# Optimization experiments

Hardware: AMD Instinct MI355X
Metric: run time of the kernel (lower is better)

Reference implementation:

```python
import jax, jax.numpy as jnp
import numpy as np

HOPS = 3
VOCAB = 100000
E = 128   # embedding_dim == hidden_size
H = 128
B = 16
S = 2048  # memory slots
M = 4     # tokens per memory cell
NE = 4000 # lang.n_entities
NR = 200  # lang.n_relations
PAD = 1   # PAD_token


def _linear_params(key, out_dim, in_dim):
    kw, kb = jax.random.split(key)
    lim = 1.0 / np.sqrt(in_dim)
    W = jax.random.uniform(kw, (out_dim, in_dim), jnp.float32, -lim, lim)
    b = jax.random.uniform(kb, (out_dim,), jnp.float32, -lim, lim)
    return W, b


def setup_inputs():
    key = jax.random.key(0)
    ks = jax.random.split(key, 10)
    story = jax.random.randint(ks[0], (B, S, M), 0, VOCAB)
    lengths = jax.random.randint(ks[1], (B,), S // 2, S + 1)
    hidden = jax.random.normal(ks[2], (B, H), jnp.float32)
    global_pointer = jax.random.uniform(ks[3], (B, S), dtype=jnp.float32)
    # (hops+1) memory embedding tables, N(0, 0.1), padding row zeroed
    C = jax.random.normal(ks[4], (HOPS + 1, VOCAB, E), jnp.float32) * 0.1
    C = C.at[:, PAD, :].set(0.0)
    Wm, Wb = _linear_params(ks[5], H, H)        # self.W
    W1w, W1b = _linear_params(ks[6], 2, H)      # structure type
    W3w, W3b = _linear_params(ks[7], NE, H)     # query entity h
    W4w, W4b = _linear_params(ks[8], NR, H)     # query entity t
    return dict(story=story, lengths=lengths, hidden=hidden,
                global_pointer=global_pointer, C=C,
                Wm=Wm, Wb=Wb, W1w=W1w, W1b=W1b,
                W3w=W3w, W3b=W3b, W4w=W4w, W4b=W4b,
                is_decoding=0)


def gumbel_hard(logits, key, tau=1.0):
    u = jax.random.uniform(key, logits.shape, logits.dtype, 1e-10, 1.0)
    g = -jnp.log(-jnp.log(u))
    y = jax.nn.softmax((logits + g) / tau, axis=-1)
    hard = jax.nn.one_hot(jnp.argmax(y, axis=-1), y.shape[-1], dtype=y.dtype)
    # straight-through estimator
    return hard - jax.lax.stop_gradient(y) + y


def reference(story, lengths, hidden, global_pointer, C,
              Wm, Wb, W1w, W1b, W3w, W3b, W4w, W4b, is_decoding):
    del global_pointer, is_decoding  # decoding branch not exercised (is_decoding=False)
    h = hidden @ Wm.T + Wb  # [B, H]

    gkey = jax.random.key(42)
    k1, k2, k3 = jax.random.split(gkey, 3)
    sp = h @ W1w.T + W1b
    sp_action = gumbel_hard(sp, k1)
    qh = h @ W3w.T + W3b
    qh_action = gumbel_hard(qh, k2)
    qt = h @ W4w.T + W4b
    qt_action = gumbel_hard(qt, k3)

    # multi-hop memory attention (dropout in eval mode -> identity)
    u = h
    prob_logit = None
    for hop in range(HOPS):
        embed_A = jnp.take(C[hop], story, axis=0).sum(axis=2)      # [B,S,E]
        prob_logit = jnp.einsum('bse,be->bs', embed_A, u)          # [B,S]
        prob = jax.nn.softmax(prob_logit, axis=1)
        embed_C = jnp.take(C[hop + 1], story, axis=0).sum(axis=2)  # [B,S,E]
        u = u + jnp.einsum('bse,bs->be', embed_C, prob)

    ret = jax.nn.sigmoid(prob_logit)
    mask = jnp.arange(S)[None, :] < lengths[:, None]
    masked_prob = jnp.where(mask, ret, 0.0)
    return (sp, sp_action, qh, qh_action, qt, qt_action, masked_prob)
```

## Files before the change

### kernel.cpp

```cpp
#include <hip/hip_runtime.h>
#include <hip/hip_bf16.h>
#include <stdint.h>

typedef __hip_bfloat16 bf16;

#define VOCABN 100000
#define EDIM 128
#define BN 16
#define SN 2048

#define H_OFF    0
#define U_OFF    2048
#define L0_OFF   4096
#define DUP_OFF  36864
#define PBV_OFF  69648
#define PBI_OFF  70848
#define G_OFF    73728

__host__ __device__ inline void tf2x32(uint32_t k0, uint32_t k1,
                                       uint32_t x0, uint32_t x1,
                                       uint32_t* o0, uint32_t* o1) {
  const uint32_t rotA[4] = {13u, 15u, 26u, 6u};
  const uint32_t rotB[4] = {17u, 29u, 16u, 24u};
  uint32_t ks0 = k0, ks1 = k1, ks2 = k0 ^ k1 ^ 0x1BD11BDAu;
  x0 += ks0; x1 += ks1;
#pragma unroll
  for (int g = 0; g < 5; ++g) {
    const uint32_t* r = (g & 1) ? rotB : rotA;
#pragma unroll
    for (int i = 0; i < 4; ++i) {
      x0 += x1;
      x1 = (x1 << r[i]) | (x1 >> (32u - r[i]));
      x1 ^= x0;
    }
    uint32_t a0 = (g % 3 == 0) ? ks1 : ((g % 3 == 1) ? ks2 : ks0);
    uint32_t a1 = (g % 3 == 0) ? ks2 : ((g % 3 == 1) ? ks0 : ks1);
    x0 += a0;
    x1 += a1 + (uint32_t)(g + 1);
  }
  *o0 = x0; *o1 = x1;
}

__device__ inline float blo(uint32_t v) { return __uint_as_float(v << 16); }
__device__ inline float bhi(uint32_t v) { return __uint_as_float(v & 0xffff0000u); }
__device__ inline uint16_t f2bu(float f) {
  bf16 h = __float2bfloat16(f);
  uint16_t u; __builtin_memcpy(&u, &h, 2); return u;
}
__device__ inline float gumbel(uint32_t ka, uint32_t kb, uint32_t flat) {
  uint32_t o0, o1;
  tf2x32(ka, kb, 0u, flat, &o0, &o1);
  uint32_t bits = o0 ^ o1;
  float u0 = __uint_as_float((bits >> 9) | 0x3f800000u) - 1.0f;
  float uu = fmaxf(1e-10f, u0 + 1e-10f);
  return -logf(-logf(uu));
}

__global__ void k_h(const float* __restrict__ hidden, const float* __restrict__ Wm,
                    const float* __restrict__ Wb, float* __restrict__ h,
                    float* __restrict__ u) {
  int b = blockIdx.x, j = threadIdx.x;
  const float4* wr = (const float4*)(Wm + (size_t)j * EDIM);
  const float4* hr = (const float4*)(hidden + (size_t)b * EDIM);
  float acc = Wb[j];
#pragma unroll
  for (int i = 0; i < 32; ++i) {
    float4 w4 = wr[i], h4 = hr[i];
    acc += w4.x * h4.x + w4.y * h4.y + w4.z * h4.z + w4.w * h4.w;
  }
  h[b * EDIM + j] = acc;
  u[b * EDIM + j] = acc;
}

__global__ void k_heads(const float* __restrict__ h,
                        const float* __restrict__ W1w, const float* __restrict__ W1b,
                        const float* __restrict__ W3w, const float* __restrict__ W3b,
                        const float* __restrict__ W4w, const float* __restrict__ W4b,
                        float* __restrict__ out, float* __restrict__ pbv,
                        int* __restrict__ pbi,
                        uint32_t k0a, uint32_t k0b, uint32_t k1a, uint32_t k1b,
                        uint32_t k2a, uint32_t k2b) {
  int bid = blockIdx.x, tid = threadIdx.x;
  __shared__ float hb[EDIM];
  __shared__ float sv[256];
  __shared__ int si[256];
  int head, b2, base, cnt, chunk, N;
  const float *W, *bias; size_t lg_off; uint32_t ka, kb;
  if (bid < 400)      { head = 1; b2 = bid / 25; chunk = bid % 25; base = chunk * 160; cnt = 160;
                        W = W3w; bias = W3b; N = 4000; lg_off = 64;     ka = k1a; kb = k1b; }
  else if (bid < 416) { head = 2; b2 = bid - 400; chunk = 0; base = 0; cnt = 200;
                        W = W4w; bias = W4b; N = 200;  lg_off = 128064; ka = k2a; kb = k2b; }
  else                { head = 0; b2 = bid - 416; chunk = 0; base = 0; cnt = 2;
                        W = W1w; bias = W1b; N = 2;    lg_off = 0;      ka = k0a; kb = k0b; }
  if (tid < 128) hb[tid] = h[b2 * EDIM + tid];
  __syncthreads();
  float best = -INFINITY; int bi = 0x7FFFFFFF;
  if (tid < cnt) {
    int c = base + tid;
    const float4* wr = (const float4*)(W + (size_t)c * EDIM);
    const float4* hb4 = (const float4*)hb;
    float acc = bias[c];
#pragma unroll
    for (int i = 0; i < 32; ++i) {
      float4 w4 = wr[i], h4 = hb4[i];
      acc += w4.x * h4.x + w4.y * h4.y + w4.z * h4.z + w4.w * h4.w;
    }
    out[lg_off + (size_t)b2 * N + c] = acc;
    best = acc + gumbel(ka, kb, (uint32_t)(b2 * N + c));
    bi = c;
  }
  sv[tid] = best; si[tid] = bi;
  __syncthreads();
  for (int s2 = 128; s2 > 0; s2 >>= 1) {
    if (tid < s2) {
      float ov = sv[tid + s2]; int oi = si[tid + s2];
      if (ov > sv[tid] || (ov == sv[tid] && oi < si[tid])) { sv[tid] = ov; si[tid] = oi; }
    }
    __syncthreads();
  }
  if (tid == 0) {
    pbv[(head * 16 + b2) * 25 + chunk] = sv[0];
    pbi[(head * 16 + b2) * 25 + chunk] = si[0];
  }
}

__global__ void k_onehot(const float* __restrict__ pbv, const int* __restrict__ pbi,
                         float* __restrict__ out) {
  int g = blockIdx.x * 256 + threadIdx.x;
  if (g >= 67232) return;
  int head, b2, c; size_t off; int nch;
  if (g < 64000)      { head = 1; b2 = g / 4000; c = g % 4000; off = 64064 + g;          nch = 25; }
  else if (g < 67200) { int gg = g - 64000; head = 2; b2 = gg / 200; c = gg % 200; off = 131264 + gg; nch = 1; }
  else                { int gg = g - 67200; head = 0; b2 = gg >> 1; c = gg & 1;   off = 32 + gg;     nch = 1; }
  float bv = -INFINITY; int bi = 0x7FFFFFFF;
  for (int ch = 0; ch < nch; ++ch) {
    float v = pbv[(head * 16 + b2) * 25 + ch];
    int i2 = pbi[(head * 16 + b2) * 25 + ch];
    if (v > bv || (v == bv && i2 < bi)) { bv = v; bi = i2; }
  }
  out[off] = (c == bi) ? 1.0f : 0.0f;
}

__global__ void k_gather_l0(const int* __restrict__ story, const float* __restrict__ C,
                            const float* __restrict__ u, uint32_t* __restrict__ G,
                            float* __restrict__ l0) {
  int wid = (blockIdx.x << 2) | (threadIdx.x >> 6);
  int lane = threadIdx.x & 63;
  int t = wid >> 15;
  int bs = wid & 32767;
  int4 idx = ((const int4*)story)[bs];
  const float2* r0 = (const float2*)(C + ((size_t)t * VOCABN + idx.x) * EDIM);
  const float2* r1 = (const float2*)(C + ((size_t)t * VOCABN + idx.y) * EDIM);
  const float2* r2 = (const float2*)(C + ((size_t)t * VOCABN + idx.z) * EDIM);
  const float2* r3 = (const float2*)(C + ((size_t)t * VOCABN + idx.w) * EDIM);
  float2 a = r0[lane], b = r1[lane], c = r2[lane], d = r3[lane];
  float lo = a.x + b.x + c.x + d.x;
  float hi = a.y + b.y + c.y + d.y;
  if (t == 0) {
    float2 uu = ((const float2*)(u + ((bs >> 11) << 7)))[lane];
    float s = lo * uu.x + hi * uu.y;
#pragma unroll
    for (int off = 32; off > 0; off >>= 1) s += __shfl_xor(s, off, 64);
    if (lane == 0) l0[bs] = s;
  } else {
    G[((size_t)(t - 1) * BN * SN + bs) * 64 + lane] =
        (uint32_t)f2bu(lo) | ((uint32_t)f2bu(hi) << 16);
  }
}

__global__ void __launch_bounds__(256) k_hopB(const uint32_t* __restrict__ Gt,
                                              const float* __restrict__ row_in,
                                              float* __restrict__ dup) {
  const int b = blockIdx.x >> 4, k = blockIdx.x & 15;
  const int tid = threadIdx.x, wave = tid >> 6, lane = tid & 63;
  __shared__ float sr[SN];
  __shared__ float red[4];
  __shared__ float acc[4][EDIM];

  const float4* rin = (const float4*)(row_in + (size_t)b * SN);
  float4* sr4 = (float4*)sr;
  for (int i = tid; i < SN / 4; i += 256) sr4[i] = rin[i];
  __syncthreads();

  float m = -INFINITY;
  for (int i = tid; i < SN; i += 256) m = fmaxf(m, sr[i]);
#pragma unroll
  for (int off = 32; off > 0; off >>= 1) m = fmaxf(m, __shfl_xor(m, off, 64));
  if (lane == 0) red[wave] = m;
  __syncthreads();
  m = fmaxf(fmaxf(red[0], red[1]), fmaxf(red[2], red[3]));

  float s = 0.f;
  for (int i = tid; i < SN; i += 256) s += expf(sr[i] - m);
#pragma unroll
  for (int off = 32; off > 0; off >>= 1) s += __shfl_xor(s, off, 64);
  __syncthreads();
  if (lane == 0) red[wave] = s;
  __syncthreads();
  float invS = 1.0f / (red[0] + red[1] + red[2] + red[3]);

  const uint32_t* Gb = Gt + (size_t)b * SN * 64;
  int sub = lane >> 4, le = lane & 15;
  float a[8] = {0, 0, 0, 0, 0, 0, 0, 0};
#pragma unroll
  for (int it = 0; it < 8; ++it) {
    int cell = k * 128 + wave * 32 + it * 4 + sub;
    uint4 v = *(const uint4*)(Gb + (size_t)cell * 64 + le * 4);
    float pp = expf(sr[cell] - m);
    a[0] += blo(v.x) * pp; a[1] += bhi(v.x) * pp;
    a[2] += blo(v.y) * pp; a[3] += bhi(v.y) * pp;
    a[4] += blo(v.z) * pp; a[5] += bhi(v.z) * pp;
    a[6] += blo(v.w) * pp; a[7] += bhi(v.w) * pp;
  }
#pragma unroll
  for (int j = 0; j < 8; ++j) {
    a[j] += __shfl_xor(a[j], 16, 64);
    a[j] += __shfl_xor(a[j], 32, 64);
  }
  if (lane < 16) {
#pragma unroll
    for (int j = 0; j < 8; ++j) acc[wave][lane * 8 + j] = a[j];
  }
  __syncthreads();
  if (tid < EDIM) {
    float d = (acc[0][tid] + acc[1][tid] + acc[2][tid] + acc[3][tid]) * invS;
    dup[((size_t)b * 16 + k) * EDIM + tid] = d;
  }
}

__global__ void __launch_bounds__(256) k_hopC(const uint32_t* __restrict__ Gt,
                                              const float* __restrict__ dup,
                                              const float* __restrict__ u_in,
                                              float* __restrict__ u_out,
                                              float* __restrict__ row_out,
                                              const int* __restrict__ lengths,
                                              float* __restrict__ out) {
  const int b = blockIdx.x >> 4, k = blockIdx.x & 15;
  const int tid = threadIdx.x, wave = tid >> 6, lane = tid & 63;
  __shared__ float u_l[EDIM];
  if (tid < EDIM) {
    float v = u_in[b * EDIM + tid];
    const float* dp = dup + (size_t)b * 16 * EDIM + tid;
#pragma unroll
    for (int kk = 0; kk < 16; ++kk) v += dp[kk * EDIM];
    u_l[tid] = v;
    if (u_out != nullptr && k == 0) u_out[b * EDIM + tid] = v;
  }
  __syncthreads();

  const uint32_t* Gb = Gt + (size_t)b * SN * 64;
  int sub = lane >> 4, le = lane & 15;
  const float4* u4 = (const float4*)u_l;
  float4 ua = u4[le * 2], ub = u4[le * 2 + 1];
  int len = (lengths != nullptr) ? lengths[b] : 0;
#pragma unroll
  for (int it = 0; it < 8; ++it) {
    int cell = k * 128 + wave * 32 + it * 4 + sub;
    uint4 v = *(const uint4*)(Gb + (size_t)cell * 64 + le * 4);
    float s = blo(v.x) * ua.x + bhi(v.x) * ua.y + blo(v.y) * ua.z + bhi(v.y) * ua.w
            + blo(v.z) * ub.x + bhi(v.z) * ub.y + blo(v.w) * ub.z + bhi(v.w) * ub.w;
#pragma unroll
    for (int off = 8; off > 0; off >>= 1) s += __shfl_xor(s, off, 64);
    if (le == 0) {
      if (row_out != nullptr) {
        row_out[(size_t)b * SN + cell] = s;
      } else {
        out[134464 + (size_t)b * SN + cell] =
            (cell < len) ? 1.0f / (1.0f + expf(-s)) : 0.0f;
      }
    }
  }
}

extern "C" void kernel_launch(void* const* d_in, const int* in_sizes, int n_in,
                              void* d_out, int out_size, void* d_ws, size_t ws_size,
                              hipStream_t stream) {
  const int *story = nullptr, *lengths = nullptr;
  const float *hidden = nullptr, *C = nullptr, *Wm = nullptr, *Wb = nullptr,
              *W1w = nullptr, *W1b = nullptr, *W3w = nullptr, *W3b = nullptr,
              *W4w = nullptr, *W4b = nullptr;
  for (int i = 0; i < n_in; ++i) {
    switch (in_sizes[i]) {
      case 16 * 2048 * 4:    story   = (const int*)d_in[i]; break;
      case 16:               lengths = (const int*)d_in[i]; break;
      case 16 * 128:         hidden  = (const float*)d_in[i]; break;
      case 4 * 100000 * 128: C       = (const float*)d_in[i]; break;
      case 128 * 128:        Wm      = (const float*)d_in[i]; break;
      case 128:              Wb      = (const float*)d_in[i]; break;
      case 2 * 128:          W1w     = (const float*)d_in[i]; break;
      case 2:                W1b     = (const float*)d_in[i]; break;
      case 4000 * 128:       W3w     = (const float*)d_in[i]; break;
      case 4000:             W3b     = (const float*)d_in[i]; break;
      case 200 * 128:        W4w     = (const float*)d_in[i]; break;
      case 200:              W4b     = (const float*)d_in[i]; break;
      default: break;
    }
  }
  float* out = (float*)d_out;
  float* ws  = (float*)d_ws;
  float* h   = ws + H_OFF;
  float* u   = ws + U_OFF;
  float* row = ws + L0_OFF;
  float* dup = ws + DUP_OFF;
  float* pbv = ws + PBV_OFF;
  int*   pbi = (int*)(ws + PBI_OFF);
  uint32_t* G = (uint32_t*)(ws + G_OFF);
  const size_t TSZ = (size_t)BN * SN * 64;

  uint32_t k0a, k0b, k1a, k1b, k2a, k2b;
  tf2x32(0u, 42u, 0u, 0u, &k0a, &k0b);
  tf2x32(0u, 42u, 0u, 1u, &k1a, &k1b);
  tf2x32(0u, 42u, 0u, 2u, &k2a, &k2b);

  k_h<<<BN, 128, 0, stream>>>(hidden, Wm, Wb, h, u);
  k_heads<<<432, 256, 0, stream>>>(h, W1w, W1b, W3w, W3b, W4w, W4b,
                                   out, pbv, pbi, k0a, k0b, k1a, k1b, k2a, k2b);
  k_onehot<<<263, 256, 0, stream>>>(pbv, pbi, out);
  k_gather_l0<<<3 * BN * SN / 4, 256, 0, stream>>>(story, C, u, G, row);

  k_hopB<<<BN * 16, 256, 0, stream>>>(G, row, dup);
  k_hopC<<<BN * 16, 256, 0, stream>>>(G, dup, u, h, row,
                                      nullptr, out);
  k_hopB<<<BN * 16, 256, 0, stream>>>(G + TSZ, row, dup);
  k_hopC<<<BN * 16, 256, 0, stream>>>(G + TSZ, dup, h, nullptr, nullptr,
                                      lengths, out);
}
```

Baseline: 332.9 us.

## Replace per-slot embedding gathers with vocab-wide dot products and scatter-weighted reductions

```diff
diff --git a/kernel.cpp b/kernel.cpp
--- a/kernel.cpp
+++ b/kernel.cpp
@@ -1,21 +1,23 @@
 #include <hip/hip_runtime.h>
 #include <hip/hip_bf16.h>
 #include <stdint.h>
-
-typedef __hip_bfloat16 bf16;
 
 #define VOCABN 100000
 #define EDIM 128
 #define BN 16
 #define SN 2048
+#define VPB 128
+#define NBV 782
 
 #define H_OFF    0
-#define U_OFF    2048
-#define L0_OFF   4096
-#define DUP_OFF  36864
-#define PBV_OFF  69648
-#define PBI_OFF  70848
-#define G_OFF    73728
+#define U0_OFF   2048
+#define U1_OFF   4096
+#define DU_OFF   6144
+#define PS_OFF   10240
+#define PBV_OFF  10368
+#define PBI_OFF  11568
+#define DT_OFF   16384
+#define WT_OFF   1616384
 
 __host__ __device__ inline void tf2x32(uint32_t k0, uint32_t k1,
                                        uint32_t x0, uint32_t x1,
@@ -41,12 +43,6 @@
   *o0 = x0; *o1 = x1;
 }
 
-__device__ inline float blo(uint32_t v) { return __uint_as_float(v << 16); }
-__device__ inline float bhi(uint32_t v) { return __uint_as_float(v & 0xffff0000u); }
-__device__ inline uint16_t f2bu(float f) {
-  bf16 h = __float2bfloat16(f);
-  uint16_t u; __builtin_memcpy(&u, &h, 2); return u;
-}
 __device__ inline float gumbel(uint32_t ka, uint32_t kb, uint32_t flat) {
   uint32_t o0, o1;
   tf2x32(ka, kb, 0u, flat, &o0, &o1);
@@ -141,135 +137,139 @@
   out[off] = (c == bi) ? 1.0f : 0.0f;
 }
 
-__global__ void k_gather_l0(const int* __restrict__ story, const float* __restrict__ C,
-                            const float* __restrict__ u, uint32_t* __restrict__ G,
-                            float* __restrict__ l0) {
-  int wid = (blockIdx.x << 2) | (threadIdx.x >> 6);
-  int lane = threadIdx.x & 63;
-  int t = wid >> 15;
-  int bs = wid & 32767;
-  int4 idx = ((const int4*)story)[bs];
-  const float2* r0 = (const float2*)(C + ((size_t)t * VOCABN + idx.x) * EDIM);
-  const float2* r1 = (const float2*)(C + ((size_t)t * VOCABN + idx.y) * EDIM);
-  const float2* r2 = (const float2*)(C + ((size_t)t * VOCABN + idx.z) * EDIM);
-  const float2* r3 = (const float2*)(C + ((size_t)t * VOCABN + idx.w) * EDIM);
-  float2 a = r0[lane], b = r1[lane], c = r2[lane], d = r3[lane];
-  float lo = a.x + b.x + c.x + d.x;
-  float hi = a.y + b.y + c.y + d.y;
-  if (t == 0) {
-    float2 uu = ((const float2*)(u + ((bs >> 11) << 7)))[lane];
-    float s = lo * uu.x + hi * uu.y;
-#pragma unroll
-    for (int off = 32; off > 0; off >>= 1) s += __shfl_xor(s, off, 64);
-    if (lane == 0) l0[bs] = s;
-  } else {
-    G[((size_t)(t - 1) * BN * SN + bs) * 64 + lane] =
-        (uint32_t)f2bu(lo) | ((uint32_t)f2bu(hi) << 16);
-  }
-}
-
-__global__ void __launch_bounds__(256) k_hopB(const uint32_t* __restrict__ Gt,
-                                              const float* __restrict__ row_in,
-                                              float* __restrict__ dup) {
-  const int b = blockIdx.x >> 4, k = blockIdx.x & 15;
-  const int tid = threadIdx.x, wave = tid >> 6, lane = tid & 63;
-  __shared__ float sr[SN];
+__global__ void __launch_bounds__(256) k_D(const float* __restrict__ Ct,
+                                           const float* __restrict__ u_in,
+                                           const float* __restrict__ du,
+                                           const float* __restrict__ ps,
+                                           int use_du,
+                                           float* __restrict__ u_out,
+                                           float* __restrict__ Dt,
+                                           float* __restrict__ wtz,
+                                           float* __restrict__ duz) {
+  __shared__ __align__(16) float u_s[16][132];
+  __shared__ __align__(16) float r_s[16][132];
+  const int bid = blockIdx.x, tid = threadIdx.x;
+
+  if (wtz) {
+    for (int i = bid * 256 + tid; i < VOCABN * 16; i += NBV * 256) wtz[i] = 0.f;
+  }
+  if (duz && bid == 0) {
+    for (int i = tid; i < 4096; i += 256) duz[i] = 0.f;
+  }
+
+  for (int i = tid; i < 2048; i += 256) {
+    int b = i >> 7, e = i & 127;
+    float v = u_in[i];
+    if (use_du) {
+      float S = 0.f;
+#pragma unroll
+      for (int sl = 0; sl < 8; ++sl) S += ps[b * 8 + sl];
+      v += du[i] * (1.0f / S);
+    }
+    u_s[b][e] = v;
+    if (u_out && bid == 0) u_out[i] = v;
+  }
+
+  const int v0 = bid * VPB;
+  const int vl = tid >> 4, b = tid & 15;
+  for (int r = 0; r < VPB / 16; ++r) {
+    int vr0 = v0 + r * 16;
+    __syncthreads();
+    for (int i = tid; i < 512; i += 256) {
+      int row = i >> 5, c4 = i & 31;
+      float4 val = make_float4(0.f, 0.f, 0.f, 0.f);
+      if (vr0 + row < VOCABN)
+        val = ((const float4*)(Ct + (size_t)(vr0 + row) * EDIM))[c4];
+      *(float4*)&r_s[row][c4 * 4] = val;
+    }
+    __syncthreads();
+    float acc = 0.f;
+    const float4* rr = (const float4*)&r_s[vl][0];
+    const float4* uu = (const float4*)&u_s[b][0];
+#pragma unroll
+    for (int i = 0; i < 32; ++i) {
+      float4 a = rr[i], c = uu[i];
+      acc += a.x * c.x + a.y * c.y + a.z * c.z + a.w * c.w;
+    }
+    int v = vr0 + vl;
+    if (v < VOCABN) Dt[(size_t)v * 16 + b] = acc;
+  }
+}
+
+__global__ void __launch_bounds__(256) k_lscat(const int* __restrict__ story,
+                                               const float* __restrict__ Dt,
+                                               float* __restrict__ wt,
+                                               float* __restrict__ ps) {
+  const int bid = blockIdx.x, tid = threadIdx.x;
+  const int b = bid >> 3, sl = bid & 7;
+  const int s = sl * 256 + tid;
+  const int wave = tid >> 6, lane = tid & 63;
+  int4 tk = ((const int4*)story)[b * SN + s];
+  float l = Dt[(size_t)tk.x * 16 + b] + Dt[(size_t)tk.y * 16 + b]
+          + Dt[(size_t)tk.z * 16 + b] + Dt[(size_t)tk.w * 16 + b];
+  float e = expf(l);
+  atomicAdd(&wt[(size_t)tk.x * 16 + b], e);
+  atomicAdd(&wt[(size_t)tk.y * 16 + b], e);
+  atomicAdd(&wt[(size_t)tk.z * 16 + b], e);
+  atomicAdd(&wt[(size_t)tk.w * 16 + b], e);
+  float sum = e;
+#pragma unroll
+  for (int off = 32; off > 0; off >>= 1) sum += __shfl_xor(sum, off, 64);
   __shared__ float red[4];
-  __shared__ float acc[4][EDIM];
-
-  const float4* rin = (const float4*)(row_in + (size_t)b * SN);
-  float4* sr4 = (float4*)sr;
-  for (int i = tid; i < SN / 4; i += 256) sr4[i] = rin[i];
+  if (lane == 0) red[wave] = sum;
   __syncthreads();
-
-  float m = -INFINITY;
-  for (int i = tid; i < SN; i += 256) m = fmaxf(m, sr[i]);
-#pragma unroll
-  for (int off = 32; off > 0; off >>= 1) m = fmaxf(m, __shfl_xor(m, off, 64));
-  if (lane == 0) red[wave] = m;
-  __syncthreads();
-  m = fmaxf(fmaxf(red[0], red[1]), fmaxf(red[2], red[3]));
-
-  float s = 0.f;
-  for (int i = tid; i < SN; i += 256) s += expf(sr[i] - m);
-#pragma unroll
-  for (int off = 32; off > 0; off >>= 1) s += __shfl_xor(s, off, 64);
-  __syncthreads();
-  if (lane == 0) red[wave] = s;
-  __syncthreads();
-  float invS = 1.0f / (red[0] + red[1] + red[2] + red[3]);
-
-  const uint32_t* Gb = Gt + (size_t)b * SN * 64;
-  int sub = lane >> 4, le = lane & 15;
-  float a[8] = {0, 0, 0, 0, 0, 0, 0, 0};
-#pragma unroll
-  for (int it = 0; it < 8; ++it) {
-    int cell = k * 128 + wave * 32 + it * 4 + sub;
-    uint4 v = *(const uint4*)(Gb + (size_t)cell * 64 + le * 4);
-    float pp = expf(sr[cell] - m);
-    a[0] += blo(v.x) * pp; a[1] += bhi(v.x) * pp;
-    a[2] += blo(v.y) * pp; a[3] += bhi(v.y) * pp;
-    a[4] += blo(v.z) * pp; a[5] += bhi(v.z) * pp;
-    a[6] += blo(v.w) * pp; a[7] += bhi(v.w) * pp;
-  }
-#pragma unroll
-  for (int j = 0; j < 8; ++j) {
-    a[j] += __shfl_xor(a[j], 16, 64);
-    a[j] += __shfl_xor(a[j], 32, 64);
-  }
-  if (lane < 16) {
-#pragma unroll
-    for (int j = 0; j < 8; ++j) acc[wave][lane * 8 + j] = a[j];
-  }
-  __syncthreads();
-  if (tid < EDIM) {
-    float d = (acc[0][tid] + acc[1][tid] + acc[2][tid] + acc[3][tid]) * invS;
-    dup[((size_t)b * 16 + k) * EDIM + tid] = d;
-  }
-}
-
-__global__ void __launch_bounds__(256) k_hopC(const uint32_t* __restrict__ Gt,
-                                              const float* __restrict__ dup,
-                                              const float* __restrict__ u_in,
-                                              float* __restrict__ u_out,
-                                              float* __restrict__ row_out,
+  if (tid == 0) ps[b * 8 + sl] = red[0] + red[1] + red[2] + red[3];
+}
+
+__global__ void __launch_bounds__(256) k_du(const float* __restrict__ Ct,
+                                            const float* __restrict__ wt,
+                                            float* __restrict__ du) {
+  __shared__ __align__(16) float r_s[16][132];
+  __shared__ float w_s[16][17];
+  const int bid = blockIdx.x, tid = threadIdx.x;
+  const int b = tid >> 4, e8 = (tid & 15) * 8;
+  float acc[8] = {0.f, 0.f, 0.f, 0.f, 0.f, 0.f, 0.f, 0.f};
+  const int v0 = bid * VPB;
+  for (int r = 0; r < VPB / 16; ++r) {
+    int vr0 = v0 + r * 16;
+    __syncthreads();
+    for (int i = tid; i < 512; i += 256) {
+      int row = i >> 5, c4 = i & 31;
+      float4 val = make_float4(0.f, 0.f, 0.f, 0.f);
+      if (vr0 + row < VOCABN)
+        val = ((const float4*)(Ct + (size_t)(vr0 + row) * EDIM))[c4];
+      *(float4*)&r_s[row][c4 * 4] = val;
+    }
+    {
+      int row = tid >> 4, bb = tid & 15;
+      w_s[row][bb] = (vr0 + row < VOCABN) ? wt[(size_t)(vr0 + row) * 16 + bb] : 0.f;
+    }
+    __syncthreads();
+#pragma unroll
+    for (int v = 0; v < 16; ++v) {
+      float w = w_s[v][b];
+      const float4* rp = (const float4*)&r_s[v][e8];
+      float4 A = rp[0], Bv = rp[1];
+      acc[0] += w * A.x;  acc[1] += w * A.y;  acc[2] += w * A.z;  acc[3] += w * A.w;
+      acc[4] += w * Bv.x; acc[5] += w * Bv.y; acc[6] += w * Bv.z; acc[7] += w * Bv.w;
+    }
+  }
+#pragma unroll
+  for (int j = 0; j < 8; ++j) atomicAdd(&du[b * EDIM + e8 + j], acc[j]);
+}
+
+__global__ void __launch_bounds__(256) k_lfin(const int* __restrict__ story,
+                                              const float* __restrict__ Dt,
                                               const int* __restrict__ lengths,
                                               float* __restrict__ out) {
-  const int b = blockIdx.x >> 4, k = blockIdx.x & 15;
-  const int tid = threadIdx.x, wave = tid >> 6, lane = tid & 63;
-  __shared__ float u_l[EDIM];
-  if (tid < EDIM) {
-    float v = u_in[b * EDIM + tid];
-    const float* dp = dup + (size_t)b * 16 * EDIM + tid;
-#pragma unroll
-    for (int kk = 0; kk < 16; ++kk) v += dp[kk * EDIM];
-    u_l[tid] = v;
-    if (u_out != nullptr && k == 0) u_out[b * EDIM + tid] = v;
-  }
-  __syncthreads();
-
-  const uint32_t* Gb = Gt + (size_t)b * SN * 64;
-  int sub = lane >> 4, le = lane & 15;
-  const float4* u4 = (const float4*)u_l;
-  float4 ua = u4[le * 2], ub = u4[le * 2 + 1];
-  int len = (lengths != nullptr) ? lengths[b] : 0;
-#pragma unroll
-  for (int it = 0; it < 8; ++it) {
-    int cell = k * 128 + wave * 32 + it * 4 + sub;
-    uint4 v = *(const uint4*)(Gb + (size_t)cell * 64 + le * 4);
-    float s = blo(v.x) * ua.x + bhi(v.x) * ua.y + blo(v.y) * ua.z + bhi(v.y) * ua.w
-            + blo(v.z) * ub.x + bhi(v.z) * ub.y + blo(v.w) * ub.z + bhi(v.w) * ub.w;
-#pragma unroll
-    for (int off = 8; off > 0; off >>= 1) s += __shfl_xor(s, off, 64);
-    if (le == 0) {
-      if (row_out != nullptr) {
-        row_out[(size_t)b * SN + cell] = s;
-      } else {
-        out[134464 + (size_t)b * SN + cell] =
-            (cell < len) ? 1.0f / (1.0f + expf(-s)) : 0.0f;
-      }
-    }
-  }
+  const int bid = blockIdx.x, tid = threadIdx.x;
+  const int b = bid >> 3, sl = bid & 7;
+  const int s = sl * 256 + tid;
+  int4 tk = ((const int4*)story)[b * SN + s];
+  float l = Dt[(size_t)tk.x * 16 + b] + Dt[(size_t)tk.y * 16 + b]
+          + Dt[(size_t)tk.z * 16 + b] + Dt[(size_t)tk.w * 16 + b];
+  int len = lengths[b];
+  out[134464 + (size_t)b * SN + s] = (s < len) ? 1.0f / (1.0f + expf(-l)) : 0.0f;
 }
 
 extern "C" void kernel_launch(void* const* d_in, const int* in_sizes, int n_in,
@@ -299,29 +299,35 @@
   float* out = (float*)d_out;
   float* ws  = (float*)d_ws;
   float* h   = ws + H_OFF;
-  float* u   = ws + U_OFF;
-  float* row = ws + L0_OFF;
-  float* dup = ws + DUP_OFF;
+  float* u0  = ws + U0_OFF;
+  float* u1  = ws + U1_OFF;
+  float* du  = ws + DU_OFF;
+  float* ps  = ws + PS_OFF;
   float* pbv = ws + PBV_OFF;
   int*   pbi = (int*)(ws + PBI_OFF);
-  uint32_t* G = (uint32_t*)(ws + G_OFF);
-  const size_t TSZ = (size_t)BN * SN * 64;
+  float* Dt  = ws + DT_OFF;
+  float* wt  = ws + WT_OFF;
+
+  const float* C0 = C;
+  const float* C1 = C + (size_t)1 * VOCABN * EDIM;
+  const float* C2 = C + (size_t)2 * VOCABN * EDIM;
 
   uint32_t k0a, k0b, k1a, k1b, k2a, k2b;
   tf2x32(0u, 42u, 0u, 0u, &k0a, &k0b);
   tf2x32(0u, 42u, 0u, 1u, &k1a, &k1b);
   tf2x32(0u, 42u, 0u, 2u, &k2a, &k2b);
 
-  k_h<<<BN, 128, 0, stream>>>(hidden, Wm, Wb, h, u);
+  k_h<<<BN, 128, 0, stream>>>(hidden, Wm, Wb, h, u0);
   k_heads<<<432, 256, 0, stream>>>(h, W1w, W1b, W3w, W3b, W4w, W4b,
                                    out, pbv, pbi, k0a, k0b, k1a, k1b, k2a, k2b);
   k_onehot<<<263, 256, 0, stream>>>(pbv, pbi, out);
-  k_gather_l0<<<3 * BN * SN / 4, 256, 0, stream>>>(story, C, u, G, row);
-
-  k_hopB<<<BN * 16, 256, 0, stream>>>(G, row, dup);
-  k_hopC<<<BN * 16, 256, 0, stream>>>(G, dup, u, h, row,
-                                      nullptr, out);
-  k_hopB<<<BN * 16, 256, 0, stream>>>(G + TSZ, row, dup);
-  k_hopC<<<BN * 16, 256, 0, stream>>>(G + TSZ, dup, h, nullptr, nullptr,
-                                      lengths, out);
-}
+
+  k_D<<<NBV, 256, 0, stream>>>(C0, u0, nullptr, nullptr, 0, nullptr, Dt, wt, du);
+  k_lscat<<<128, 256, 0, stream>>>(story, Dt, wt, ps);
+  k_du<<<NBV, 256, 0, stream>>>(C1, wt, du);
+  k_D<<<NBV, 256, 0, stream>>>(C1, u0, du, ps, 1, u1, Dt, wt, nullptr);
+  k_lscat<<<128, 256, 0, stream>>>(story, Dt, wt, ps);
+  k_du<<<NBV, 256, 0, stream>>>(C2, wt, du + 2048);
+  k_D<<<NBV, 256, 0, stream>>>(C2, u1, du + 2048, ps, 1, nullptr, Dt, nullptr, nullptr);
+  k_lfin<<<128, 256, 0, stream>>>(story, Dt, lengths, out);
+}
```

Measured after the change: 717.7 us. 116% more time.
